# Kernel optimization log

Measured on AMD Instinct MI355X. Metric: run time of the kernel, lower is better.

The kernel has to match this reference:

```python
import jax, jax.numpy as jnp
import numpy as np

N = 256      # n_tokens
N_OUT = 128  # n_out
B = 128
D = 64


def setup_inputs() -> dict:
    key = jax.random.key(0)
    k1, k2 = jax.random.split(key)
    k = jax.random.normal(k1, (B, N, D), dtype=jnp.float32)
    v = jax.random.normal(k2, (B, N, D), dtype=jnp.float32)
    return {"k": k, "v": v}


def _greedy_merge(k, v, n, n_out):
    b = k.shape[0]
    r = n - n_out
    ti, tj = jnp.triu_indices(n, 1)  # row-major upper-triangle pairs, [m]
    m = ti.shape[0]
    b_rge = jnp.arange(b)

    # cosine-similarity scores on the upper triangle
    kn = k / jnp.linalg.norm(k, axis=-1, keepdims=True)
    scores = jnp.einsum('bnd,bmd->bnm', kn, kn)
    scores_tri = scores[:, ti, tj]                       # [b, m]
    sort_scores = jnp.argsort(-scores_tri, axis=-1, stable=True)  # descending
    ijs = jnp.stack([ti, tj], axis=-1)                   # [m, 2]
    sorted_ijs = ijs[sort_scores]                        # [b, m, 2]

    def body(carry, _):
        groups, group_ids, sorted_masks = carry
        # first still-valid (unsuppressed) pair per batch element
        sel = jnp.argmax(sorted_masks, axis=1)           # [b]
        ij = sorted_ijs[b_rge, sel]                      # [b, 2]
        i = group_ids[b_rge, ij[:, 0]]                   # current group of token i0
        j = group_ids[b_rge, ij[:, 1]]                   # current group of token j0
        group_i = groups[b_rge, i]                       # [b, n] bool membership
        # merge group i into group j
        groups = groups.at[b_rge, j].set(groups[b_rge, j] | group_i)
        group_ids = jnp.where(group_i, j[:, None], group_ids)
        groups = groups.at[b_rge, i].set(False)
        # suppress all intra-group-j edges
        group_j = groups[b_rge, j]                       # [b, n]
        edges_tri = jnp.take(group_j, ti, axis=1) & jnp.take(group_j, tj, axis=1)  # [b, m]
        perm = jnp.take_along_axis(edges_tri, sort_scores, axis=1)
        sorted_masks = sorted_masks & ~perm
        return (groups, group_ids, sorted_masks), None

    groups0 = jnp.tile(jnp.eye(n, dtype=bool), (b, 1, 1))
    group_ids0 = jnp.tile(jnp.arange(n, dtype=jnp.int32), (b, 1))
    masks0 = jnp.ones((b, m), dtype=bool)
    (groups, _, _), _ = jax.lax.scan(body, (groups0, group_ids0, masks0), None, length=r)

    # keep the n_out surviving (non-empty) group rows, preserving row order
    alive = groups.any(-1)                                       # [b, n]
    keep = jnp.argsort(~alive, axis=1, stable=True)[:, :n_out]   # [b, n_out]
    groups = jnp.take_along_axis(groups, keep[:, :, None], axis=1)  # [b, n_out, n]
    group_sizes = groups.sum(-1)                                 # [b, n_out] int
    out = jnp.einsum('bon,bnd->bod',
                     groups / group_sizes[..., None].astype(jnp.float32), v)
    return out, group_sizes


def reference(k, v):
    return _greedy_merge(k, v, N, N_OUT)
```

## Files before the change

### kernel.cpp

```cpp
#include <hip/hip_runtime.h>
#include <stdint.h>

#define NTOK 256
#define NOUT 128
#define DIM 64
#define NB 128
#define LCAP 768
#define KTOT 1536
#define SCAP 2048
#define PCAP 1024
#define NMERGE 128
#define KAPPA 0.24f
#define SCREEN 0.2395f
#define NTILES84 1056
#define TILES_PER_SUB84 528

__device__ __forceinline__ unsigned mono_f32(float s) {
  unsigned u = __float_as_uint(s);
  return (u & 0x80000000u) ? ~u : (u | 0x80000000u);
}

__device__ __forceinline__ unsigned long long shflx64(unsigned long long x, int m) {
  unsigned lo = (unsigned)x, hi = (unsigned)(x >> 32);
  lo = __shfl_xor(lo, m);
  hi = __shfl_xor(hi, m);
  return ((unsigned long long)hi << 32) | lo;
}

__device__ __forceinline__ void tile84(int T, int& tio, int& tjo) {
  float tf = (65.0f - sqrtf(4225.0f - 4.0f * (float)T)) * 0.5f;
  int t = (int)tf;
  if (t < 0) t = 0;
  if (t > 31) t = 31;
  while (t < 31 && 65 * (t + 1) - (t + 1) * (t + 1) <= T) ++t;
  while (t > 0 && 65 * t - t * t > T) --t;
  tio = t;
  tjo = 2 * t + (T - (65 * t - t * t));
}

#define CEX(a, b, up)                         \
  do {                                        \
    unsigned long long _a = (a), _b = (b);    \
    bool _sw = (up) ? (_a < _b) : (_a > _b);  \
    if (_sw) { (a) = _b; (b) = _a; }          \
  } while (0)

#define KEEP(v, o, km) ((km) ? ((v) > (o) ? (v) : (o)) : ((v) < (o) ? (v) : (o)))

__device__ __forceinline__ void normalize_to_knT(const float* __restrict__ K,
                                                 float* __restrict__ knT,
                                                 int b, int tid) {
  const int t = tid >> 1, h = tid & 1;
  const float* kp = K + ((size_t)b * NTOK + t) * DIM + h * 32;
  double ss = 0.0;
  float vals[32];
#pragma unroll
  for (int q = 0; q < 8; ++q) {
    float4 v4 = *reinterpret_cast<const float4*>(kp + q * 4);
    vals[q * 4 + 0] = v4.x; vals[q * 4 + 1] = v4.y;
    vals[q * 4 + 2] = v4.z; vals[q * 4 + 3] = v4.w;
    ss += (double)v4.x * v4.x + (double)v4.y * v4.y +
          (double)v4.z * v4.z + (double)v4.w * v4.w;
  }
  double other = __shfl_xor(ss, 1);
  double nrm = sqrt(ss + other);
#pragma unroll
  for (int q = 0; q < 32; ++q)
    knT[(h * 32 + q) * NTOK + t] = (float)((double)vals[q] / nrm);
}

#define SMEM_A 75808
__global__ __launch_bounds__(512) void gm_gram(const float* __restrict__ K,
                                               unsigned* __restrict__ gcnt,
                                               unsigned long long* __restrict__ gkeys) {
  extern __shared__ char smem[];
  float* knT = (float*)smem;
  unsigned* lpairs = (unsigned*)(smem + 65536);
  unsigned long long* lkeys = (unsigned long long*)(smem + 69632);
  int* lmisc = (int*)(smem + 75776);

  const int tid = threadIdx.x;
  const int b = blockIdx.x >> 1, sub = blockIdx.x & 1;

  if (tid == 0) { lmisc[0] = 0; lmisc[1] = 0; }

  normalize_to_knT(K, knT, b, tid);
  __syncthreads();

  const int base = sub * TILES_PER_SUB84;
  for (int t = tid; t < TILES_PER_SUB84; t += 512) {
    int ti, tj;
    tile84(base + t, ti, tj);
    const int i0 = ti * 8, j0 = tj * 4;

    float acc[8][4] = {};
#pragma unroll 4
    for (int d = 0; d < 64; ++d) {
      const float* row = knT + d * NTOK;
      const float4 a0 = *reinterpret_cast<const float4*>(row + i0);
      const float4 a1 = *reinterpret_cast<const float4*>(row + i0 + 4);
      const float4 bv = *reinterpret_cast<const float4*>(row + j0);
      const float aa[8] = {a0.x, a0.y, a0.z, a0.w, a1.x, a1.y, a1.z, a1.w};
      const float bb[4] = {bv.x, bv.y, bv.z, bv.w};
#pragma unroll
      for (int r = 0; r < 8; ++r)
#pragma unroll
        for (int c = 0; c < 4; ++c)
          acc[r][c] = fmaf(aa[r], bb[c], acc[r][c]);
    }
#pragma unroll
    for (int r = 0; r < 8; ++r)
#pragma unroll
      for (int c = 0; c < 4; ++c) {
        const int i = i0 + r, j = j0 + c;
        if (i < j && acc[r][c] >= SCREEN) {
          const int idx = atomicAdd(&lmisc[0], 1);
          if (idx < PCAP) lpairs[idx] = (unsigned)((i << 8) | j);
        }
      }
  }
  __syncthreads();

  const int npRaw = lmisc[0];
  const int np = npRaw > PCAP ? PCAP : npRaw;
  for (int e = tid; e < np; e += 512) {
    const unsigned p = lpairs[e];
    const int i = (int)(p >> 8), j = (int)(p & 255u);
    double s = 0.0;
    for (int d = 0; d < 64; ++d)
      s = fma((double)knT[d * NTOK + i], (double)knT[d * NTOK + j], s);
    const float sf = (float)s;
    if (sf >= KAPPA) {
      const unsigned long long key =
          ((unsigned long long)mono_f32(sf) << 16) |
          (unsigned)(65535 - ((i << 8) | j));
      const int idx = atomicAdd(&lmisc[1], 1);
      if (idx < LCAP) lkeys[idx] = key;
    }
  }
  __syncthreads();

  const int nkRaw = lmisc[1];
  if (tid == 0)
    gcnt[2 * b + sub] = (npRaw > PCAP) ? 0x7FFFFFFFu : (unsigned)nkRaw;
  const int nk = nkRaw > LCAP ? LCAP : nkRaw;
  unsigned long long* seg = gkeys + (size_t)b * KTOT + (size_t)sub * LCAP;
  for (int e = tid; e < nk; e += 512) seg[e] = lkeys[e];
}

#define SMEM_W 85600
__global__ __launch_bounds__(512) void gm_walk(const float* __restrict__ K,
                                               const float* __restrict__ V,
                                               float* __restrict__ OUT,
                                               const unsigned* __restrict__ gcnt,
                                               const unsigned long long* __restrict__ gkeys) {
  extern __shared__ char smem[];
  float* knT = (float*)smem;
  float* accO = (float*)smem;
  unsigned long long* keys = (unsigned long long*)(smem + 65536);
  int* gid = (int*)(smem + 81920);
  int* cnt256 = (int*)(smem + 82944);
  int* scn = (int*)(smem + 83968);
  int* rep = (int*)(smem + 84992);
  int* misc = (int*)(smem + 85504);
  unsigned long long* red = (unsigned long long*)(smem + 85520);
  unsigned long long* bkey = (unsigned long long*)(smem + 85584);

  const int tid = threadIdx.x;
  const int lane = tid & 63;
  const int wid = tid >> 6;
  const int b = blockIdx.x;

  const unsigned n0 = gcnt[2 * b], n1 = gcnt[2 * b + 1];
  const bool fullFB = (n0 > LCAP) || (n1 > LCAP);
  const int n0c = n0 > LCAP ? LCAP : (int)n0;
  const int n1c = n1 > LCAP ? LCAP : (int)n1;
  const int cntC = n0c + n1c;

  if (tid == 0) misc[3] = fullFB ? 0 : NMERGE;
  if (tid < NTOK) gid[tid] = tid;

  {
    const unsigned long long* gk = gkeys + (size_t)b * KTOT;
    for (int e = tid; e < SCAP; e += 512) {
      unsigned long long v = 0ULL;
      if (e < KTOT) {
        const int seg = e / LCAP, off = e - seg * LCAP;
        const int lim = seg ? n1c : n0c;
        if (off < lim) v = gk[e];
      }
      keys[e] = v;
    }
  }
  __syncthreads();

  {
    const int e0 = 4 * tid;
    unsigned long long v0 = keys[e0], v1 = keys[e0 + 1],
                       v2 = keys[e0 + 2], v3 = keys[e0 + 3];
    for (int kk = 2; kk <= SCAP; kk <<= 1) {
      for (int jj = kk >> 1; jj > 0; jj >>= 1) {
        if (jj >= 256) {
          __syncthreads();
          keys[e0] = v0; keys[e0 + 1] = v1; keys[e0 + 2] = v2; keys[e0 + 3] = v3;
          __syncthreads();
          const int p0 = e0 ^ jj;
          unsigned long long o0 = keys[p0], o1 = keys[p0 + 1],
                             o2 = keys[p0 + 2], o3 = keys[p0 + 3];
          const bool km = ((e0 & kk) == 0) == ((e0 & jj) == 0);
          v0 = KEEP(v0, o0, km); v1 = KEEP(v1, o1, km);
          v2 = KEEP(v2, o2, km); v3 = KEEP(v3, o3, km);
        } else if (jj >= 4) {
          const int m = jj >> 2;
          unsigned long long o0 = shflx64(v0, m), o1 = shflx64(v1, m),
                             o2 = shflx64(v2, m), o3 = shflx64(v3, m);
          const bool km = ((e0 & kk) == 0) == ((e0 & jj) == 0);
          v0 = KEEP(v0, o0, km); v1 = KEEP(v1, o1, km);
          v2 = KEEP(v2, o2, km); v3 = KEEP(v3, o3, km);
        } else if (jj == 2) {
          const bool up = ((e0 & kk) == 0);
          CEX(v0, v2, up); CEX(v1, v3, up);
        } else {
          bool up0, up1;
          if (kk == 2) { up0 = true; up1 = false; }
          else { up0 = up1 = ((e0 & kk) == 0); }
          CEX(v0, v1, up0); CEX(v2, v3, up1);
        }
      }
    }
    __syncthreads();
    keys[e0] = v0; keys[e0 + 1] = v1; keys[e0 + 2] = v2; keys[e0 + 3] = v3;
  }
  __syncthreads();

  if (!fullFB && wid == 0) {
    int rg0 = lane, rg1 = 64 + lane, rg2 = 128 + lane, rg3 = 192 + lane;
    int done = 0;
    for (int cursor = 0; cursor < cntC && done < NMERGE; cursor += 64) {
      const int idx = cursor + lane;
      const unsigned long long key = (idx < cntC) ? keys[idx] : 0ULL;
      const int pi = 255 - (int)((key >> 8) & 255);
      const int pj = 255 - (int)(key & 255);
      const int sli = pi & 63, ssi = pi >> 6;
      const int slj = pj & 63, ssj = pj >> 6;
      const int a0 = __shfl(rg0, sli), a1 = __shfl(rg1, sli),
                a2 = __shfl(rg2, sli), a3 = __shfl(rg3, sli);
      const int b0 = __shfl(rg0, slj), b1 = __shfl(rg1, slj),
                b2 = __shfl(rg2, slj), b3 = __shfl(rg3, slj);
      int gpi = (ssi == 0) ? a0 : (ssi == 1) ? a1 : (ssi == 2) ? a2 : a3;
      int gpj = (ssj == 0) ? b0 : (ssj == 1) ? b1 : (ssj == 2) ? b2 : b3;
      if (key == 0ULL) { gpi = 0; gpj = 0; }
      for (;;) {
        const unsigned long long mask = __ballot(gpi != gpj);
        if (!mask) break;
        const int f = __ffsll((long long)mask) - 1;
        const int gi = __shfl(gpi, f), gj = __shfl(gpj, f);
        if (lane == f) gpi = gpj;
        if (gpi == gi) gpi = gj;
        if (gpj == gi) gpj = gj;
        if (rg0 == gi) rg0 = gj;
        if (rg1 == gi) rg1 = gj;
        if (rg2 == gi) rg2 = gj;
        if (rg3 == gi) rg3 = gj;
        if (++done == NMERGE) break;
      }
    }
    gid[lane] = rg0; gid[64 + lane] = rg1;
    gid[128 + lane] = rg2; gid[192 + lane] = rg3;
    if (lane == 0) misc[3] = done;
  }
  __syncthreads();

  {
    const int start = misc[3];
    if (start < NMERGE) {
      normalize_to_knT(K, knT, b, tid);
      __syncthreads();
      for (int mg = start; mg < NMERGE; ++mg) {
        unsigned long long best = 0ULL;
        const int p = tid >> 2, q = tid & 3;
        const int jA = 128 + p, jB = 127 - p;
        const int lenA = jA;
        const int s0 = q * 64, s1 = (q == 3) ? 255 : (q * 64 + 64);
        for (int e = s0; e < s1; ++e) {
          const int i = (e < lenA) ? e : (e - lenA);
          const int j = (e < lenA) ? jA : jB;
          if (gid[i] != gid[j]) {
            double s = 0.0;
            for (int d = 0; d < 64; ++d)
              s = fma((double)knT[d * NTOK + i], (double)knT[d * NTOK + j], s);
            const unsigned long long key =
                ((unsigned long long)mono_f32((float)s) << 16) |
                (unsigned)(65535 - ((i << 8) | j));
            if (key > best) best = key;
          }
        }
#pragma unroll
        for (int off = 32; off; off >>= 1) {
          unsigned long long o = __shfl_down(best, off);
          if (o > best) best = o;
        }
        if (lane == 0) red[wid] = best;
        __syncthreads();
        if (tid == 0) {
          unsigned long long mx = red[0];
          for (int w = 1; w < 8; ++w)
            if (red[w] > mx) mx = red[w];
          bkey[0] = mx;
        }
        __syncthreads();
        const unsigned long long bk = bkey[0];
        const int pi = 255 - (int)((bk >> 8) & 255);
        const int pj = 255 - (int)(bk & 255);
        const int gi = gid[pi], gj = gid[pj];
        __syncthreads();
        if (tid < NTOK && gid[tid] == gi) gid[tid] = gj;
        __syncthreads();
      }
    }
  }
  __syncthreads();

  if (tid < NTOK) cnt256[tid] = 0;
  for (int e = tid; e < NOUT * DIM; e += 512) accO[e] = 0.0f;
  __syncthreads();
  if (tid < NTOK) atomicAdd(&cnt256[gid[tid]], 1);
  __syncthreads();
  if (wid == 0) {
    const int t4 = lane * 4;
    const int c0 = cnt256[t4 + 0] != 0, c1 = cnt256[t4 + 1] != 0,
              c2 = cnt256[t4 + 2] != 0, c3 = cnt256[t4 + 3] != 0;
    const int tot = c0 + c1 + c2 + c3;
    int run = tot;
#pragma unroll
    for (int off = 1; off < 64; off <<= 1) {
      int o = __shfl_up(run, off);
      if (lane >= off) run += o;
    }
    const int bs = run - tot;
    scn[t4 + 0] = bs + c0;
    scn[t4 + 1] = bs + c0 + c1;
    scn[t4 + 2] = bs + c0 + c1 + c2;
    scn[t4 + 3] = bs + tot;
  }
  __syncthreads();
  if (tid < NTOK && cnt256[tid]) rep[scn[tid] - 1] = tid;
  __syncthreads();

  {
    const int t = tid >> 1, h = tid & 1;
    const int slot = scn[gid[t]] - 1;
    const float* vp = V + ((size_t)b * NTOK + t) * DIM + h * 32;
    float* dst = accO + slot * DIM + h * 32;
#pragma unroll
    for (int q = 0; q < 8; ++q) {
      float4 v4 = *reinterpret_cast<const float4*>(vp + q * 4);
      atomicAdd(&dst[q * 4 + 0], v4.x);
      atomicAdd(&dst[q * 4 + 1], v4.y);
      atomicAdd(&dst[q * 4 + 2], v4.z);
      atomicAdd(&dst[q * 4 + 3], v4.w);
    }
  }
  __syncthreads();

  float* outMain = OUT + (size_t)b * (NOUT * DIM);
  for (int e = tid; e < NOUT * DIM; e += 512) {
    const int o = e >> 6;
    const float sz = (float)cnt256[rep[o]];
    outMain[e] = accO[e] / sz;
  }
  float* outSz = OUT + (size_t)NB * NOUT * DIM + (size_t)b * NOUT;
  for (int o = tid; o < NOUT; o += 512) outSz[o] = (float)cnt256[rep[o]];
}

#define FCAP 1024
#define SMEM_F 83584
__global__ __launch_bounds__(512) void gm_fused(const float* __restrict__ K,
                                                const float* __restrict__ V,
                                                float* __restrict__ OUT) {
  extern __shared__ char smem[];
  float* knT = (float*)smem;
  float* accO = (float*)smem;
  unsigned long long* keys = (unsigned long long*)(smem + 65536);
  unsigned* lpairs = (unsigned*)(smem + 73728);
  int* gid = (int*)(smem + 77824);
  int* cnt256 = (int*)(smem + 80896);
  int* scn = (int*)(smem + 81920);
  int* rep = (int*)(smem + 82944);
  unsigned long long* red = (unsigned long long*)(smem + 83456);
  unsigned long long* bkey = (unsigned long long*)(smem + 83520);
  int* misc = (int*)(smem + 83528);

  const int tid = threadIdx.x;
  const int lane = tid & 63;
  const int wid = tid >> 6;
  const int b = blockIdx.x;

  if (tid == 0) { misc[0] = 0; misc[1] = 0; }
  if (tid < NTOK) gid[tid] = tid;

  normalize_to_knT(K, knT, b, tid);
  __syncthreads();

  for (int t = tid; t < NTILES84; t += 512) {
    int ti, tj;
    tile84(t, ti, tj);
    const int i0 = ti * 8, j0 = tj * 4;
    float acc[8][4] = {};
#pragma unroll 4
    for (int d = 0; d < 64; ++d) {
      const float* row = knT + d * NTOK;
      const float4 a0 = *reinterpret_cast<const float4*>(row + i0);
      const float4 a1 = *reinterpret_cast<const float4*>(row + i0 + 4);
      const float4 bv = *reinterpret_cast<const float4*>(row + j0);
      const float aa[8] = {a0.x, a0.y, a0.z, a0.w, a1.x, a1.y, a1.z, a1.w};
      const float bb[4] = {bv.x, bv.y, bv.z, bv.w};
#pragma unroll
      for (int r = 0; r < 8; ++r)
#pragma unroll
        for (int c = 0; c < 4; ++c)
          acc[r][c] = fmaf(aa[r], bb[c], acc[r][c]);
    }
#pragma unroll
    for (int r = 0; r < 8; ++r)
#pragma unroll
      for (int c = 0; c < 4; ++c) {
        const int i = i0 + r, j = j0 + c;
        if (i < j && acc[r][c] >= SCREEN) {
          const int idx = atomicAdd(&misc[0], 1);
          if (idx < PCAP) lpairs[idx] = (unsigned)((i << 8) | j);
        }
      }
  }
  __syncthreads();

  const int npRaw = misc[0];
  const int np = npRaw > PCAP ? PCAP : npRaw;
  const bool fullFB = (npRaw > PCAP);
  for (int e = tid; e < np; e += 512) {
    const unsigned p = lpairs[e];
    const int i = (int)(p >> 8), j = (int)(p & 255u);
    double s = 0.0;
    for (int d = 0; d < 64; ++d)
      s = fma((double)knT[d * NTOK + i], (double)knT[d * NTOK + j], s);
    const float sf = (float)s;
    if (sf >= KAPPA) {
      const unsigned long long key =
          ((unsigned long long)mono_f32(sf) << 16) |
          (unsigned)(65535 - ((i << 8) | j));
      const int idx = atomicAdd(&misc[1], 1);
      keys[idx] = key;
    }
  }
  if (tid == 0) misc[3] = fullFB ? 0 : NMERGE;
  __syncthreads();
  const int nk = misc[1];

  {
    const int e0 = 2 * tid;
    unsigned long long v0 = (e0 + 0 < nk) ? keys[e0 + 0] : 0ULL;
    unsigned long long v1 = (e0 + 1 < nk) ? keys[e0 + 1] : 0ULL;
    for (int kk = 2; kk <= FCAP; kk <<= 1) {
      for (int jj = kk >> 1; jj > 0; jj >>= 1) {
        if (jj >= 128) {
          __syncthreads();
          keys[e0] = v0; keys[e0 + 1] = v1;
          __syncthreads();
          const int p0 = e0 ^ jj;
          const unsigned long long o0 = keys[p0], o1 = keys[p0 + 1];
          const bool km = ((e0 & kk) == 0) == ((e0 & jj) == 0);
          v0 = KEEP(v0, o0, km); v1 = KEEP(v1, o1, km);
        } else if (jj >= 2) {
          const int m = jj >> 1;
          const unsigned long long o0 = shflx64(v0, m), o1 = shflx64(v1, m);
          const bool km = ((e0 & kk) == 0) == ((e0 & jj) == 0);
          v0 = KEEP(v0, o0, km); v1 = KEEP(v1, o1, km);
        } else {
          const bool up = ((e0 & kk) == 0);
          CEX(v0, v1, up);
        }
      }
    }
    __syncthreads();
    keys[e0] = v0; keys[e0 + 1] = v1;
  }
  __syncthreads();

  if (!fullFB && wid == 0) {
    int rg0 = lane, rg1 = 64 + lane, rg2 = 128 + lane, rg3 = 192 + lane;
    int done = 0;
    for (int cursor = 0; cursor < nk && done < NMERGE; cursor += 64) {
      const int idx = cursor + lane;
      const unsigned long long key = (idx < nk) ? keys[idx] : 0ULL;
      const int pi = 255 - (int)((key >> 8) & 255);
      const int pj = 255 - (int)(key & 255);
      const int sli = pi & 63, ssi = pi >> 6;
      const int slj = pj & 63, ssj = pj >> 6;
      const int a0 = __shfl(rg0, sli), a1 = __shfl(rg1, sli),
                a2 = __shfl(rg2, sli), a3 = __shfl(rg3, sli);
      const int b0 = __shfl(rg0, slj), b1 = __shfl(rg1, slj),
                b2 = __shfl(rg2, slj), b3 = __shfl(rg3, slj);
      int gpi = (ssi == 0) ? a0 : (ssi == 1) ? a1 : (ssi == 2) ? a2 : a3;
      int gpj = (ssj == 0) ? b0 : (ssj == 1) ? b1 : (ssj == 2) ? b2 : b3;
      if (key == 0ULL) { gpi = 0; gpj = 0; }
      for (;;) {
        const unsigned long long mask = __ballot(gpi != gpj);
        if (!mask) break;
        const int f = __ffsll((long long)mask) - 1;
        const int gi = __shfl(gpi, f), gj = __shfl(gpj, f);
        if (lane == f) gpi = gpj;
        if (gpi == gi) gpi = gj;
        if (gpj == gi) gpj = gj;
        if (rg0 == gi) rg0 = gj;
        if (rg1 == gi) rg1 = gj;
        if (rg2 == gi) rg2 = gj;
        if (rg3 == gi) rg3 = gj;
        if (++done == NMERGE) break;
      }
    }
    gid[lane] = rg0; gid[64 + lane] = rg1;
    gid[128 + lane] = rg2; gid[192 + lane] = rg3;
    if (lane == 0) misc[3] = done;
  }
  __syncthreads();

  {
    const int start = misc[3];
    for (int mg = start; mg < NMERGE; ++mg) {
      unsigned long long best = 0ULL;
      const int p = tid >> 2, q = tid & 3;
      const int jA = 128 + p, jB = 127 - p;
      const int lenA = jA;
      const int s0 = q * 64, s1 = (q == 3) ? 255 : (q * 64 + 64);
      for (int e = s0; e < s1; ++e) {
        const int i = (e < lenA) ? e : (e - lenA);
        const int j = (e < lenA) ? jA : jB;
        if (gid[i] != gid[j]) {
          double s = 0.0;
          for (int d = 0; d < 64; ++d)
            s = fma((double)knT[d * NTOK + i], (double)knT[d * NTOK + j], s);
          const unsigned long long key =
              ((unsigned long long)mono_f32((float)s) << 16) |
              (unsigned)(65535 - ((i << 8) | j));
          if (key > best) best = key;
        }
      }
#pragma unroll
      for (int off = 32; off; off >>= 1) {
        unsigned long long o = __shfl_down(best, off);
        if (o > best) best = o;
      }
      if (lane == 0) red[wid] = best;
      __syncthreads();
      if (tid == 0) {
        unsigned long long mx = red[0];
        for (int w = 1; w < 8; ++w)
          if (red[w] > mx) mx = red[w];
        bkey[0] = mx;
      }
      __syncthreads();
      const unsigned long long bk = bkey[0];
      const int pi = 255 - (int)((bk >> 8) & 255);
      const int pj = 255 - (int)(bk & 255);
      const int gi = gid[pi], gj = gid[pj];
      __syncthreads();
      if (tid < NTOK && gid[tid] == gi) gid[tid] = gj;
      __syncthreads();
    }
  }
  __syncthreads();

  if (tid < NTOK) cnt256[tid] = 0;
  for (int e = tid; e < NOUT * DIM; e += 512) accO[e] = 0.0f;
  __syncthreads();
  if (tid < NTOK) atomicAdd(&cnt256[gid[tid]], 1);
  __syncthreads();
  if (wid == 0) {
    const int t4 = lane * 4;
    const int c0 = cnt256[t4 + 0] != 0, c1 = cnt256[t4 + 1] != 0,
              c2 = cnt256[t4 + 2] != 0, c3 = cnt256[t4 + 3] != 0;
    const int tot = c0 + c1 + c2 + c3;
    int run = tot;
#pragma unroll
    for (int off = 1; off < 64; off <<= 1) {
      int o = __shfl_up(run, off);
      if (lane >= off) run += o;
    }
    const int bs = run - tot;
    scn[t4 + 0] = bs + c0;
    scn[t4 + 1] = bs + c0 + c1;
    scn[t4 + 2] = bs + c0 + c1 + c2;
    scn[t4 + 3] = bs + tot;
  }
  __syncthreads();
  if (tid < NTOK && cnt256[tid]) rep[scn[tid] - 1] = tid;
  __syncthreads();

  {
    const int t = tid >> 1, h = tid & 1;
    const int slot = scn[gid[t]] - 1;
    const float* vp = V + ((size_t)b * NTOK + t) * DIM + h * 32;
    float* dst = accO + slot * DIM + h * 32;
#pragma unroll
    for (int q = 0; q < 8; ++q) {
      float4 v4 = *reinterpret_cast<const float4*>(vp + q * 4);
      atomicAdd(&dst[q * 4 + 0], v4.x);
      atomicAdd(&dst[q * 4 + 1], v4.y);
      atomicAdd(&dst[q * 4 + 2], v4.z);
      atomicAdd(&dst[q * 4 + 3], v4.w);
    }
  }
  __syncthreads();

  float* outMain = OUT + (size_t)b * (NOUT * DIM);
  for (int e = tid; e < NOUT * DIM; e += 512) {
    const int o = e >> 6;
    const float sz = (float)cnt256[rep[o]];
    outMain[e] = accO[e] / sz;
  }
  float* outSz = OUT + (size_t)NB * NOUT * DIM + (size_t)b * NOUT;
  for (int o = tid; o < NOUT; o += 512) outSz[o] = (float)cnt256[rep[o]];
}

extern "C" void kernel_launch(void* const* d_in, const int* in_sizes, int n_in,
                              void* d_out, int out_size, void* d_ws, size_t ws_size,
                              hipStream_t stream) {
  const float* K = (const float*)d_in[0];
  const float* V = (const float*)d_in[1];
  float* OUT = (float*)d_out;
  (void)in_sizes; (void)n_in; (void)out_size;

  const size_t need = 1024 + (size_t)NB * KTOT * sizeof(unsigned long long);
  if (ws_size >= need) {
    unsigned* gcnt = (unsigned*)d_ws;
    unsigned long long* gkeys = (unsigned long long*)((char*)d_ws + 1024);
    hipFuncSetAttribute(reinterpret_cast<const void*>(gm_gram),
                        hipFuncAttributeMaxDynamicSharedMemorySize, SMEM_A);
    hipFuncSetAttribute(reinterpret_cast<const void*>(gm_walk),
                        hipFuncAttributeMaxDynamicSharedMemorySize, SMEM_W);
    gm_gram<<<dim3(NB * 2), dim3(512), SMEM_A, stream>>>(K, gcnt, gkeys);
    gm_walk<<<dim3(NB), dim3(512), SMEM_W, stream>>>(K, V, OUT, gcnt, gkeys);
  } else {
    hipFuncSetAttribute(reinterpret_cast<const void*>(gm_fused),
                        hipFuncAttributeMaxDynamicSharedMemorySize, SMEM_F);
    gm_fused<<<dim3(NB), dim3(512), SMEM_F, stream>>>(K, V, OUT);
  }
}
```

Measured before the change: 86.84 us.

## Split gram into four sub-blocks of 256 threads and shrink walk sort width

The Gram/screen kernel now runs four 256-thread blocks per batch instead of two 512-thread blocks. Each block normalizes all tokens (one thread per token) and handles a quarter of the tiles. The walk kernel uses 256 threads, compacts the four key segments into a dense 1024-entry buffer and bitonic-sorts 1024 keys instead of 2048. This cuts sort work and raises grid parallelism for the Gram stage. In exchange, each gram block repeats the normalization and the per-segment caps are smaller, so more batches may drop to the slow fallback path.

```diff
diff --git a/kernel.cpp b/kernel.cpp
--- a/kernel.cpp
+++ b/kernel.cpp
@@ -5,15 +5,16 @@
 #define NOUT 128
 #define DIM 64
 #define NB 128
-#define LCAP 768
+#define LCAP 384
+#define NSEG 4
 #define KTOT 1536
-#define SCAP 2048
-#define PCAP 1024
+#define WCAP 1024
+#define PCAPA 512
 #define NMERGE 128
 #define KAPPA 0.24f
 #define SCREEN 0.2395f
 #define NTILES84 1056
-#define TILES_PER_SUB84 528
+#define TILES_PER_SUB84 264
 
 __device__ __forceinline__ unsigned mono_f32(float s) {
   unsigned u = __float_as_uint(s);
@@ -47,6 +48,34 @@
 
 #define KEEP(v, o, km) ((km) ? ((v) > (o) ? (v) : (o)) : ((v) < (o) ? (v) : (o)))
 
+__device__ __forceinline__ void norm_tok(const float* __restrict__ K,
+                                         float* __restrict__ knT,
+                                         int b, int t) {
+  const float* kp = K + ((size_t)b * NTOK + t) * DIM;
+  float vals[64];
+  double s0 = 0.0, s1 = 0.0;
+#pragma unroll
+  for (int q = 0; q < 8; ++q) {
+    float4 v4 = *reinterpret_cast<const float4*>(kp + q * 4);
+    vals[q * 4 + 0] = v4.x; vals[q * 4 + 1] = v4.y;
+    vals[q * 4 + 2] = v4.z; vals[q * 4 + 3] = v4.w;
+    s0 += (double)v4.x * v4.x + (double)v4.y * v4.y +
+          (double)v4.z * v4.z + (double)v4.w * v4.w;
+  }
+#pragma unroll
+  for (int q = 8; q < 16; ++q) {
+    float4 v4 = *reinterpret_cast<const float4*>(kp + q * 4);
+    vals[q * 4 + 0] = v4.x; vals[q * 4 + 1] = v4.y;
+    vals[q * 4 + 2] = v4.z; vals[q * 4 + 3] = v4.w;
+    s1 += (double)v4.x * v4.x + (double)v4.y * v4.y +
+          (double)v4.z * v4.z + (double)v4.w * v4.w;
+  }
+  const double nrm = sqrt(s0 + s1);
+#pragma unroll
+  for (int d = 0; d < 64; ++d)
+    knT[d * NTOK + t] = (float)((double)vals[d] / nrm);
+}
+
 __device__ __forceinline__ void normalize_to_knT(const float* __restrict__ K,
                                                  float* __restrict__ knT,
                                                  int b, int tid) {
@@ -69,26 +98,25 @@
     knT[(h * 32 + q) * NTOK + t] = (float)((double)vals[q] / nrm);
 }
 
-#define SMEM_A 75808
-__global__ __launch_bounds__(512) void gm_gram(const float* __restrict__ K,
+#define SMEM_A 70672
+__global__ __launch_bounds__(256) void gm_gram(const float* __restrict__ K,
                                                unsigned* __restrict__ gcnt,
                                                unsigned long long* __restrict__ gkeys) {
   extern __shared__ char smem[];
   float* knT = (float*)smem;
   unsigned* lpairs = (unsigned*)(smem + 65536);
-  unsigned long long* lkeys = (unsigned long long*)(smem + 69632);
-  int* lmisc = (int*)(smem + 75776);
+  unsigned long long* lkeys = (unsigned long long*)(smem + 67584);
+  int* lmisc = (int*)(smem + 70656);
 
   const int tid = threadIdx.x;
-  const int b = blockIdx.x >> 1, sub = blockIdx.x & 1;
+  const int b = blockIdx.x >> 2, sub = blockIdx.x & 3;
 
   if (tid == 0) { lmisc[0] = 0; lmisc[1] = 0; }
-
-  normalize_to_knT(K, knT, b, tid);
+  norm_tok(K, knT, b, tid);
   __syncthreads();
 
   const int base = sub * TILES_PER_SUB84;
-  for (int t = tid; t < TILES_PER_SUB84; t += 512) {
+  for (int t = tid; t < TILES_PER_SUB84; t += 256) {
     int ti, tj;
     tile84(base + t, ti, tj);
     const int i0 = ti * 8, j0 = tj * 4;
@@ -115,15 +143,15 @@
         const int i = i0 + r, j = j0 + c;
         if (i < j && acc[r][c] >= SCREEN) {
           const int idx = atomicAdd(&lmisc[0], 1);
-          if (idx < PCAP) lpairs[idx] = (unsigned)((i << 8) | j);
+          if (idx < PCAPA) lpairs[idx] = (unsigned)((i << 8) | j);
         }
       }
   }
   __syncthreads();
 
   const int npRaw = lmisc[0];
-  const int np = npRaw > PCAP ? PCAP : npRaw;
-  for (int e = tid; e < np; e += 512) {
+  const int np = npRaw > PCAPA ? PCAPA : npRaw;
+  for (int e = tid; e < np; e += 256) {
     const unsigned p = lpairs[e];
     const int i = (int)(p >> 8), j = (int)(p & 255u);
     double s = 0.0;
@@ -142,14 +170,15 @@
 
   const int nkRaw = lmisc[1];
   if (tid == 0)
-    gcnt[2 * b + sub] = (npRaw > PCAP) ? 0x7FFFFFFFu : (unsigned)nkRaw;
+    gcnt[NSEG * b + sub] =
+        (npRaw > PCAPA || nkRaw > LCAP) ? 0x7FFFFFFFu : (unsigned)nkRaw;
   const int nk = nkRaw > LCAP ? LCAP : nkRaw;
   unsigned long long* seg = gkeys + (size_t)b * KTOT + (size_t)sub * LCAP;
-  for (int e = tid; e < nk; e += 512) seg[e] = lkeys[e];
-}
-
-#define SMEM_W 85600
-__global__ __launch_bounds__(512) void gm_walk(const float* __restrict__ K,
+  for (int e = tid; e < nk; e += 256) seg[e] = lkeys[e];
+}
+
+#define SMEM_W 77376
+__global__ __launch_bounds__(256) void gm_walk(const float* __restrict__ K,
                                                const float* __restrict__ V,
                                                float* __restrict__ OUT,
                                                const unsigned* __restrict__ gcnt,
@@ -158,38 +187,43 @@
   float* knT = (float*)smem;
   float* accO = (float*)smem;
   unsigned long long* keys = (unsigned long long*)(smem + 65536);
-  int* gid = (int*)(smem + 81920);
-  int* cnt256 = (int*)(smem + 82944);
-  int* scn = (int*)(smem + 83968);
-  int* rep = (int*)(smem + 84992);
-  int* misc = (int*)(smem + 85504);
-  unsigned long long* red = (unsigned long long*)(smem + 85520);
-  unsigned long long* bkey = (unsigned long long*)(smem + 85584);
+  int* gid = (int*)(smem + 73728);
+  int* cnt256 = (int*)(smem + 74752);
+  int* scn = (int*)(smem + 75776);
+  int* rep = (int*)(smem + 76800);
+  int* misc = (int*)(smem + 77312);
+  unsigned long long* red = (unsigned long long*)(smem + 77328);
+  unsigned long long* bkey = (unsigned long long*)(smem + 77360);
 
   const int tid = threadIdx.x;
   const int lane = tid & 63;
   const int wid = tid >> 6;
   const int b = blockIdx.x;
 
-  const unsigned n0 = gcnt[2 * b], n1 = gcnt[2 * b + 1];
-  const bool fullFB = (n0 > LCAP) || (n1 > LCAP);
-  const int n0c = n0 > LCAP ? LCAP : (int)n0;
-  const int n1c = n1 > LCAP ? LCAP : (int)n1;
-  const int cntC = n0c + n1c;
-
-  if (tid == 0) misc[3] = fullFB ? 0 : NMERGE;
-  if (tid < NTOK) gid[tid] = tid;
+  const unsigned m0 = gcnt[NSEG * b + 0], m1 = gcnt[NSEG * b + 1],
+                 m2 = gcnt[NSEG * b + 2], m3 = gcnt[NSEG * b + 3];
+  const bool segOVF = (m0 > LCAP) || (m1 > LCAP) || (m2 > LCAP) || (m3 > LCAP);
+  const int n0 = m0 > LCAP ? LCAP : (int)m0;
+  const int n1 = m1 > LCAP ? LCAP : (int)m1;
+  const int n2 = m2 > LCAP ? LCAP : (int)m2;
+  const int n3 = m3 > LCAP ? LCAP : (int)m3;
+  const int off1 = n0, off2 = n0 + n1, off3 = n0 + n1 + n2;
+  const int cntC = off3 + n3;
+  const bool fast = !segOVF && (cntC <= WCAP);
+
+  if (tid == 0) misc[3] = fast ? NMERGE : 0;
+  gid[tid] = tid;
 
   {
     const unsigned long long* gk = gkeys + (size_t)b * KTOT;
-    for (int e = tid; e < SCAP; e += 512) {
+    for (int dst = tid; dst < WCAP; dst += 256) {
       unsigned long long v = 0ULL;
-      if (e < KTOT) {
-        const int seg = e / LCAP, off = e - seg * LCAP;
-        const int lim = seg ? n1c : n0c;
-        if (off < lim) v = gk[e];
-      }
-      keys[e] = v;
+      if (fast && dst < cntC) {
+        const int seg = (dst >= off1) + (dst >= off2) + (dst >= off3);
+        const int base = (seg == 0) ? 0 : (seg == 1) ? off1 : (seg == 2) ? off2 : off3;
+        v = gk[seg * LCAP + (dst - base)];
+      }
+      keys[dst] = v;
     }
   }
   __syncthreads();
@@ -198,7 +232,7 @@
     const int e0 = 4 * tid;
     unsigned long long v0 = keys[e0], v1 = keys[e0 + 1],
                        v2 = keys[e0 + 2], v3 = keys[e0 + 3];
-    for (int kk = 2; kk <= SCAP; kk <<= 1) {
+    for (int kk = 2; kk <= WCAP; kk <<= 1) {
       for (int jj = kk >> 1; jj > 0; jj >>= 1) {
         if (jj >= 256) {
           __syncthreads();
@@ -233,7 +267,7 @@
   }
   __syncthreads();
 
-  if (!fullFB && wid == 0) {
+  if (fast && wid == 0) {
     int rg0 = lane, rg1 = 64 + lane, rg2 = 128 + lane, rg3 = 192 + lane;
     int done = 0;
     for (int cursor = 0; cursor < cntC && done < NMERGE; cursor += 64) {
@@ -274,14 +308,14 @@
   {
     const int start = misc[3];
     if (start < NMERGE) {
-      normalize_to_knT(K, knT, b, tid);
+      norm_tok(K, knT, b, tid);
       __syncthreads();
       for (int mg = start; mg < NMERGE; ++mg) {
         unsigned long long best = 0ULL;
-        const int p = tid >> 2, q = tid & 3;
+        const int p = tid >> 1, q = tid & 1;
         const int jA = 128 + p, jB = 127 - p;
         const int lenA = jA;
-        const int s0 = q * 64, s1 = (q == 3) ? 255 : (q * 64 + 64);
+        const int s0 = q * 128, s1 = (q == 1) ? 255 : 128;
         for (int e = s0; e < s1; ++e) {
           const int i = (e < lenA) ? e : (e - lenA);
           const int j = (e < lenA) ? jA : jB;
@@ -304,7 +338,7 @@
         __syncthreads();
         if (tid == 0) {
           unsigned long long mx = red[0];
-          for (int w = 1; w < 8; ++w)
+          for (int w = 1; w < 4; ++w)
             if (red[w] > mx) mx = red[w];
           bkey[0] = mx;
         }
@@ -314,17 +348,17 @@
         const int pj = 255 - (int)(bk & 255);
         const int gi = gid[pi], gj = gid[pj];
         __syncthreads();
-        if (tid < NTOK && gid[tid] == gi) gid[tid] = gj;
+        if (gid[tid] == gi) gid[tid] = gj;
         __syncthreads();
       }
     }
   }
   __syncthreads();
 
-  if (tid < NTOK) cnt256[tid] = 0;
-  for (int e = tid; e < NOUT * DIM; e += 512) accO[e] = 0.0f;
-  __syncthreads();
-  if (tid < NTOK) atomicAdd(&cnt256[gid[tid]], 1);
+  cnt256[tid] = 0;
+  for (int e = tid; e < NOUT * DIM; e += 256) accO[e] = 0.0f;
+  __syncthreads();
+  atomicAdd(&cnt256[gid[tid]], 1);
   __syncthreads();
   if (wid == 0) {
     const int t4 = lane * 4;
@@ -344,16 +378,15 @@
     scn[t4 + 3] = bs + tot;
   }
   __syncthreads();
-  if (tid < NTOK && cnt256[tid]) rep[scn[tid] - 1] = tid;
+  if (cnt256[tid]) rep[scn[tid] - 1] = tid;
   __syncthreads();
 
   {
-    const int t = tid >> 1, h = tid & 1;
-    const int slot = scn[gid[t]] - 1;
-    const float* vp = V + ((size_t)b * NTOK + t) * DIM + h * 32;
-    float* dst = accO + slot * DIM + h * 32;
-#pragma unroll
-    for (int q = 0; q < 8; ++q) {
+    const int slot = scn[gid[tid]] - 1;
+    const float* vp = V + ((size_t)b * NTOK + tid) * DIM;
+    float* dst = accO + slot * DIM;
+#pragma unroll
+    for (int q = 0; q < 16; ++q) {
       float4 v4 = *reinterpret_cast<const float4*>(vp + q * 4);
       atomicAdd(&dst[q * 4 + 0], v4.x);
       atomicAdd(&dst[q * 4 + 1], v4.y);
@@ -364,15 +397,16 @@
   __syncthreads();
 
   float* outMain = OUT + (size_t)b * (NOUT * DIM);
-  for (int e = tid; e < NOUT * DIM; e += 512) {
+  for (int e = tid; e < NOUT * DIM; e += 256) {
     const int o = e >> 6;
     const float sz = (float)cnt256[rep[o]];
     outMain[e] = accO[e] / sz;
   }
   float* outSz = OUT + (size_t)NB * NOUT * DIM + (size_t)b * NOUT;
-  for (int o = tid; o < NOUT; o += 512) outSz[o] = (float)cnt256[rep[o]];
-}
-
+  if (tid < NOUT) outSz[tid] = (float)cnt256[rep[tid]];
+}
+
+#define FPCAP 1024
 #define FCAP 1024
 #define SMEM_F 83584
 __global__ __launch_bounds__(512) void gm_fused(const float* __restrict__ K,
@@ -428,15 +462,15 @@
         const int i = i0 + r, j = j0 + c;
         if (i < j && acc[r][c] >= SCREEN) {
           const int idx = atomicAdd(&misc[0], 1);
-          if (idx < PCAP) lpairs[idx] = (unsigned)((i << 8) | j);
+          if (idx < FPCAP) lpairs[idx] = (unsigned)((i << 8) | j);
         }
       }
   }
   __syncthreads();
 
   const int npRaw = misc[0];
-  const int np = npRaw > PCAP ? PCAP : npRaw;
-  const bool fullFB = (npRaw > PCAP);
+  const int np = npRaw > FPCAP ? FPCAP : npRaw;
+  const bool fullFB = (npRaw > FPCAP);
   for (int e = tid; e < np; e += 512) {
     const unsigned p = lpairs[e];
     const int i = (int)(p >> 8), j = (int)(p & 255u);
@@ -486,7 +520,7 @@
   }
   __syncthreads();
 
-  if (!fullFB && wid == 0) {
+  if (misc[3] == NMERGE && wid == 0) {
     int rg0 = lane, rg1 = 64 + lane, rg2 = 128 + lane, rg3 = 192 + lane;
     int done = 0;
     for (int cursor = 0; cursor < nk && done < NMERGE; cursor += 64) {
@@ -630,16 +664,16 @@
   float* OUT = (float*)d_out;
   (void)in_sizes; (void)n_in; (void)out_size;
 
-  const size_t need = 1024 + (size_t)NB * KTOT * sizeof(unsigned long long);
+  const size_t need = 4096 + (size_t)NB * KTOT * sizeof(unsigned long long);
   if (ws_size >= need) {
     unsigned* gcnt = (unsigned*)d_ws;
-    unsigned long long* gkeys = (unsigned long long*)((char*)d_ws + 1024);
+    unsigned long long* gkeys = (unsigned long long*)((char*)d_ws + 4096);
     hipFuncSetAttribute(reinterpret_cast<const void*>(gm_gram),
                         hipFuncAttributeMaxDynamicSharedMemorySize, SMEM_A);
     hipFuncSetAttribute(reinterpret_cast<const void*>(gm_walk),
                         hipFuncAttributeMaxDynamicSharedMemorySize, SMEM_W);
-    gm_gram<<<dim3(NB * 2), dim3(512), SMEM_A, stream>>>(K, gcnt, gkeys);
-    gm_walk<<<dim3(NB), dim3(512), SMEM_W, stream>>>(K, V, OUT, gcnt, gkeys);
+    gm_gram<<<dim3(NB * 4), dim3(256), SMEM_A, stream>>>(K, gcnt, gkeys);
+    gm_walk<<<dim3(NB), dim3(256), SMEM_W, stream>>>(K, V, OUT, gcnt, gkeys);
   } else {
     hipFuncSetAttribute(reinterpret_cast<const void*>(gm_fused),
                         hipFuncAttributeMaxDynamicSharedMemorySize, SMEM_F);
```

Result: no change. 85.50 us (-1.5%).
